# Kernel tuning notes

Measured on AMD Instinct MI355X. Metric: run time of the kernel, lower is better.

The kernel has to match this reference:

```python
import jax, jax.numpy as jnp
import numpy as np

ATTN_HEADS = 4
NEG = -1e9
LN_EPS = 1e-5


def _ln(x, s, b):
    m = x.mean(-1, keepdims=True)
    v = ((x - m) ** 2).mean(-1, keepdims=True)
    return (x - m) * jax.lax.rsqrt(v + LN_EPS) * s + b


def setup_inputs() -> dict:
    key = jax.random.key(0)
    ks = jax.random.split(key, 40)
    B, L, D, FF, NL = 512, 192, 256, 1024, 2
    V, U, I = 30000, 100000, 50000
    Lp, Ln, NF = 30, 300, 13
    Lu = jax.random.randint(ks[0], (B,), 1, L // 2)
    Li = jax.random.randint(ks[1], (B,), 1, L // 2)
    inp = {
        'attr': jax.random.randint(ks[2], (B, L), 0, V),
        'attr_inds': jax.random.randint(ks[3], (B, L), 0, 3),
        'attr_tf': jax.random.uniform(ks[4], (B, L), dtype=jnp.float32),
        'attr_feat': jax.random.normal(ks[5], (B, L, NF), dtype=jnp.float32),
        'attr_lens': Lu + Li,
        'attr_lens_user': Lu,
        'attr_lens_item': Li,
        'user_ids': jax.random.randint(ks[6], (B,), 0, U),
        'item_ids': jax.random.randint(ks[7], (B,), 0, I),
        'pos_targets': jax.random.randint(ks[8], (B, Lp), 0, V),
        'pos_lens': jax.random.randint(ks[9], (B,), 1, Lp + 1),
        'neg_targets': jax.random.randint(ks[10], (B, Ln), 0, V),
        'neg_lens': jax.random.randint(ks[11], (B,), 1, Ln + 1),
        # embedding tables (uniform(-0.1,0.1) per f_init_weight)
        'attr_emb': jax.random.uniform(ks[12], (V, D), minval=-0.1, maxval=0.1),
        'ind_emb': jax.random.uniform(ks[13], (3, D), minval=-0.1, maxval=0.1),
        'user_emb_table': jax.random.uniform(ks[14], (U, D), minval=-0.1, maxval=0.1),
        'item_emb_table': jax.random.uniform(ks[15], (I, D), minval=-0.1, maxval=0.1),
        'out_emb_user': jax.random.uniform(ks[16], (V, 2 * D), minval=-0.1, maxval=0.1),
        'out_emb_item': jax.random.uniform(ks[17], (V, 2 * D), minval=-0.1, maxval=0.1),
        # attr-weight head: Linear(13,1) + sigmoid
        'feat_w': jax.random.normal(ks[18], (NF,)) * 0.02,
        'feat_b': jnp.zeros(()),
        # transformer encoder params, stacked over NL layers
        'Wqkv': jax.random.normal(ks[19], (NL, 3 * D, D)) * 0.02,
        'bqkv': jnp.zeros((NL, 3 * D)),
        'Wo': jax.random.normal(ks[20], (NL, D, D)) * 0.02,
        'bo': jnp.zeros((NL, D)),
        'ln1_s': jnp.ones((NL, D)), 'ln1_b': jnp.zeros((NL, D)),
        'W1': jax.random.normal(ks[21], (NL, FF, D)) * 0.02,
        'b1': jnp.zeros((NL, FF)),
        'W2': jax.random.normal(ks[22], (NL, D, FF)) * 0.02,
        'b2': jnp.zeros((NL, D)),
        'ln2_s': jnp.ones((NL, D)), 'ln2_b': jnp.zeros((NL, D)),
    }
    return inp


def reference(attr, attr_inds, attr_tf, attr_feat, attr_lens, attr_lens_user,
              attr_lens_item, user_ids, item_ids, pos_targets, pos_lens,
              neg_targets, neg_lens, attr_emb, ind_emb, user_emb_table,
              item_emb_table, out_emb_user, out_emb_item, feat_w, feat_b,
              Wqkv, bqkv, Wo, bo, ln1_s, ln1_b, W1, b1, W2, b2, ln2_s, ln2_b):
    B, L = attr.shape
    D = attr_emb.shape[1]
    NL = Wqkv.shape[0]
    Dh = D // ATTN_HEADS
    pos = jnp.arange(L)
    valid = pos[None, :] < attr_lens[:, None]  # [B,L] True = valid key

    x = attr_emb[attr] + ind_emb[attr_inds]  # [B,L,D]
    for l in range(NL):  # post-LN TransformerEncoderLayer, relu, no dropout
        qkv = x @ Wqkv[l].T + bqkv[l]
        q, k, v = jnp.split(qkv, 3, axis=-1)
        q = q.reshape(B, L, ATTN_HEADS, Dh).transpose(0, 2, 1, 3)
        k = k.reshape(B, L, ATTN_HEADS, Dh).transpose(0, 2, 1, 3)
        v = v.reshape(B, L, ATTN_HEADS, Dh).transpose(0, 2, 1, 3)
        scores = jnp.einsum('bhqd,bhkd->bhqk', q, k) / np.sqrt(Dh).astype(x.dtype)
        scores = jnp.where(valid[:, None, None, :], scores, NEG)
        a = jax.nn.softmax(scores, axis=-1)
        ctx = jnp.einsum('bhqk,bhkd->bhqd', a, v).transpose(0, 2, 1, 3).reshape(B, L, D)
        x = _ln(x + ctx @ Wo[l].T + bo[l], ln1_s[l], ln1_b[l])
        ff = jax.nn.relu(x @ W1[l].T + b1[l]) @ W2[l].T + b2[l]
        x = _ln(x + ff, ln2_s[l], ln2_b[l])

    # ragged weighted segment average over user span [0,Lu) and item span [Lu,Lu+Li)
    w_user = jax.nn.sigmoid(attr_feat @ feat_w + feat_b)  # [B,L]
    wted = x * attr_tf[..., None]
    umask = pos[None, :] < attr_lens_user[:, None]
    imask = (~umask) & (pos[None, :] < (attr_lens_user + attr_lens_item)[:, None])
    user_x = (wted * w_user[..., None] * umask[..., None]).sum(1) / attr_lens_user[:, None].astype(x.dtype)
    item_x = (wted * (1.0 - w_user)[..., None] * imask[..., None]).sum(1) / attr_lens_item[:, None].astype(x.dtype)

    user_out = jnp.concatenate([user_x, user_emb_table[user_ids]], axis=-1)  # [B,2D]
    item_out = jnp.concatenate([item_x, item_emb_table[item_ids]], axis=-1)

    def logit(t):
        return (jnp.einsum('bkd,bd->bk', out_emb_user[t], user_out)
                + jnp.einsum('bkd,bd->bk', out_emb_item[t], item_out))

    pos_logits = logit(pos_targets)
    neg_logits = logit(neg_targets)
    pmask = jnp.arange(pos_targets.shape[1])[None, :] < pos_lens[:, None]
    nmask = jnp.arange(neg_targets.shape[1])[None, :] < neg_lens[:, None]
    logits = jnp.concatenate([pos_logits, neg_logits], axis=-1)
    mask = jnp.concatenate([pmask, nmask], axis=-1)
    new_targets = jnp.concatenate([jnp.ones_like(pos_targets), jnp.zeros_like(neg_targets)], axis=1) * mask
    return logits, mask, new_targets
```

## Files before the change

### kernel.cpp

```cpp
#include <hip/hip_runtime.h>
#include <hip/hip_bf16.h>
#include <cstdint>
#include <cstddef>

#define B_ 512
#define L_ 192
#define D_ 256
#define H_ 4
#define DH_ 64
#define FF_ 1024
#define NL_ 2
#define LP_ 30
#define LNEG_ 300
#define NF_ 13
#define M_ (B_*L_)
#define NT_ 330
#define V_ 30000

typedef __attribute__((ext_vector_type(8))) short bf16x8;
typedef __attribute__((ext_vector_type(4))) float f32x4;

__device__ __forceinline__ ushort f2b(float f) {
  union { float f; uint32_t u; } v; v.f = f;
  uint32_t u = v.u;
  return (ushort)((u + 0x7FFFu + ((u >> 16) & 1u)) >> 16);
}
__device__ __forceinline__ float b2f(ushort u) {
  union { uint32_t u; float f; } v; v.u = (uint32_t)u << 16; return v.f;
}

__global__ __launch_bounds__(512) void k_prefix(
    const int* __restrict__ lens, int* __restrict__ off,
    int* __restrict__ ccnt, int* __restrict__ ccntp, int Bc, int nchunks)
{
  const int t = threadIdx.x;
  int s = 0;
  for (int i = 0; i < t; ++i) s += lens[i];
  off[t] = s;
  if (t == 511) off[512] = s + lens[511];
  if (t < nchunks) {
    int s2 = 0;
    const int c0 = t * Bc;
    for (int i = 0; i < Bc; ++i) s2 += lens[c0 + i];
    ccnt[t]  = s2;
    ccntp[t] = (s2 + 127) & ~127;
  }
}

__global__ __launch_bounds__(256) void k_f2b(const float* __restrict__ in, ushort* __restrict__ out) {
  const int i = (blockIdx.x*256 + threadIdx.x)*8;
  float4 a = *(const float4*)(in+i);
  float4 b = *(const float4*)(in+i+4);
  ushort4 o1; o1.x=f2b(a.x); o1.y=f2b(a.y); o1.z=f2b(a.z); o1.w=f2b(a.w);
  ushort4 o2; o2.x=f2b(b.x); o2.y=f2b(b.y); o2.z=f2b(b.z); o2.w=f2b(b.w);
  *(ushort4*)(out+i)   = o1;
  *(ushort4*)(out+i+4) = o2;
}

__global__ __launch_bounds__(256) void k_f2b4(
    const float* __restrict__ wq, const float* __restrict__ wo,
    const float* __restrict__ w1, const float* __restrict__ w2,
    ushort* __restrict__ oq, ushort* __restrict__ oo,
    ushort* __restrict__ o1, ushort* __restrict__ o2)
{
  int bb = blockIdx.x;
  const float* in; ushort* out; int base;
  if (bb < 192)      { in = wq; out = oq; base = bb; }
  else if (bb < 256) { in = wo; out = oo; base = bb - 192; }
  else if (bb < 512) { in = w1; out = o1; base = bb - 256; }
  else               { in = w2; out = o2; base = bb - 512; }
  const int i = base*2048 + threadIdx.x*8;
  float4 a = *(const float4*)(in+i);
  float4 b = *(const float4*)(in+i+4);
  ushort4 q1; q1.x=f2b(a.x); q1.y=f2b(a.y); q1.z=f2b(a.z); q1.w=f2b(a.w);
  ushort4 q2; q2.x=f2b(b.x); q2.y=f2b(b.y); q2.z=f2b(b.z); q2.w=f2b(b.w);
  *(ushort4*)(out+i)   = q1;
  *(ushort4*)(out+i+4) = q2;
}

__global__ __launch_bounds__(256) void k_embed(
    const int* __restrict__ attr, const int* __restrict__ inds,
    const int* __restrict__ lens, const int* __restrict__ off,
    const float* __restrict__ attr_emb, const float* __restrict__ ind_emb,
    ushort* __restrict__ xb)
{
  int idx = blockIdx.x*256 + threadIdx.x;
  int token = idx >> 6;
  int c = (idx & 63) * 4;
  int b = token / L_;
  int l = token - b*L_;
  if (l >= lens[b]) return;
  size_t crow = (size_t)off[b] + l;
  int a = attr[token];
  int id = inds[token];
  const float4 e  = *(const float4*)(attr_emb + (size_t)a*D_ + c);
  const float4 ie = *(const float4*)(ind_emb  + (size_t)id*D_ + c);
  ushort4 ob; ob.x=f2b(e.x+ie.x); ob.y=f2b(e.y+ie.y); ob.z=f2b(e.z+ie.z); ob.w=f2b(e.w+ie.w);
  *(ushort4*)(xb + crow*D_ + c) = ob;
}

template<int OUT_BF16, int RELU>
__global__ __launch_bounds__(256) void k_gemm_mfma(
    const ushort* __restrict__ A, const int* __restrict__ aoffp,
    const int* __restrict__ cntp,
    const ushort* __restrict__ W, const float* __restrict__ bias,
    void* __restrict__ Cv, int N, int K)
{
  if ((int)blockIdx.y * 128 >= *cntp) return;
  __shared__ alignas(16) ushort As[8192];
  __shared__ alignas(16) ushort Bs[8192];
  const int abase = *aoffp;
  const int tid = threadIdx.x;
  const int w = tid >> 6, l = tid & 63;
  const int g = l >> 4, c16 = l & 15;
  const int m0 = blockIdx.y*128, n0 = blockIdx.x*128;
  const int wr = w >> 1, wc = w & 1;
  const int swzr = (c16 & 7) << 4;

  f32x4 acc[4][4];
  #pragma unroll
  for (int i=0;i<4;++i)
    #pragma unroll
    for (int j=0;j<4;++j) acc[i][j] = (f32x4){0.f,0.f,0.f,0.f};

  for (int k0=0; k0<K; k0+=64) {
    #pragma unroll
    for (int i=0;i<4;++i) {
      const int li  = i*4096 + tid*16;
      const int row = li >> 7;
      const int col = ((li & 127) ^ ((row & 7) << 4)) >> 1;
      const ushort* ga = A + (size_t)(abase+m0+row)*K + k0 + col;
      const ushort* gb = W + (size_t)(n0+row)*K + k0 + col;
      ushort* la = As + i*2048 + w*512;
      ushort* lb = Bs + i*2048 + w*512;
      __builtin_amdgcn_global_load_lds((const __attribute__((address_space(1))) unsigned int*)ga,
                                       (__attribute__((address_space(3))) unsigned int*)la, 16, 0, 0);
      __builtin_amdgcn_global_load_lds((const __attribute__((address_space(1))) unsigned int*)gb,
                                       (__attribute__((address_space(3))) unsigned int*)lb, 16, 0, 0);
    }
    __syncthreads();
    #pragma unroll
    for (int ks=0; ks<2; ++ks) {
      const int cb = ((g*16 + ks*64) ^ swzr) >> 1;
      bf16x8 af[4], bfr[4];
      #pragma unroll
      for (int i2=0;i2<4;++i2) {
        af[i2]  = *(const bf16x8*)(As + (size_t)(wr*64 + i2*16 + c16)*64 + cb);
        bfr[i2] = *(const bf16x8*)(Bs + (size_t)(wc*64 + i2*16 + c16)*64 + cb);
      }
      #pragma unroll
      for (int mi=0;mi<4;++mi)
        #pragma unroll
        for (int ni=0;ni<4;++ni)
          acc[mi][ni] = __builtin_amdgcn_mfma_f32_16x16x32_bf16(af[mi], bfr[ni], acc[mi][ni], 0,0,0);
    }
    __syncthreads();
  }
  const int col0 = n0 + wc*64 + c16;
  const int row0 = m0 + wr*64 + (g<<2);
  #pragma unroll
  for (int ni=0;ni<4;++ni) {
    const float bv = bias[col0 + ni*16];
    #pragma unroll
    for (int mi=0;mi<4;++mi) {
      #pragma unroll
      for (int r=0;r<4;++r) {
        float v = acc[mi][ni][r] + bv;
        if (RELU) v = fmaxf(v, 0.f);
        const size_t idx = (size_t)(row0 + mi*16 + r)*N + col0 + ni*16;
        if (OUT_BF16) ((ushort*)Cv)[idx] = f2b(v);
        else          ((float*)Cv)[idx]  = v;
      }
    }
  }
}

__global__ __launch_bounds__(512) void k_gemm_ln(
    const ushort* __restrict__ A,
    const int* __restrict__ cntp, const int* __restrict__ cnt,
    const int* __restrict__ xoffp,
    const ushort* __restrict__ W,
    const float* __restrict__ bias,
    const float* __restrict__ lns, const float* __restrict__ lnb,
    ushort* __restrict__ xb, int K)
{
  const int m0 = blockIdx.x*128;
  if (m0 >= *cntp) return;
  __shared__ alignas(16) ushort As[8192];
  __shared__ alignas(16) ushort Bs[16384];
  __shared__ float red[4][2][128];
  const int tid = threadIdx.x;
  const int w = tid >> 6, l = tid & 63;
  const int g = l >> 4, c16 = l & 15;
  const int wr = w >> 2, wc = w & 3;
  const int swzr = (c16 & 7) << 4;

  f32x4 acc[4][4];
  #pragma unroll
  for (int i=0;i<4;++i)
    #pragma unroll
    for (int j=0;j<4;++j) acc[i][j] = (f32x4){0.f,0.f,0.f,0.f};

  for (int k0=0; k0<K; k0+=64) {
    #pragma unroll
    for (int i=0;i<2;++i) {
      const int li  = i*8192 + tid*16;
      const int row = li >> 7;
      const int col = ((li & 127) ^ ((row & 7) << 4)) >> 1;
      const ushort* ga = A + (size_t)(m0+row)*K + k0 + col;
      ushort* la = As + i*4096 + w*512;
      __builtin_amdgcn_global_load_lds((const __attribute__((address_space(1))) unsigned int*)ga,
                                       (__attribute__((address_space(3))) unsigned int*)la, 16, 0, 0);
    }
    #pragma unroll
    for (int i=0;i<4;++i) {
      const int li  = i*8192 + tid*16;
      const int row = li >> 7;
      const int col = ((li & 127) ^ ((row & 7) << 4)) >> 1;
      const ushort* gb = W + (size_t)row*K + k0 + col;
      ushort* lb = Bs + i*4096 + w*512;
      __builtin_amdgcn_global_load_lds((const __attribute__((address_space(1))) unsigned int*)gb,
                                       (__attribute__((address_space(3))) unsigned int*)lb, 16, 0, 0);
    }
    __syncthreads();
    #pragma unroll
    for (int ks=0; ks<2; ++ks) {
      const int cb = ((g*16 + ks*64) ^ swzr) >> 1;
      bf16x8 af[4], bfr[4];
      #pragma unroll
      for (int i2=0;i2<4;++i2) {
        af[i2]  = *(const bf16x8*)(As + (size_t)(wr*64 + i2*16 + c16)*64 + cb);
        bfr[i2] = *(const bf16x8*)(Bs + (size_t)(wc*64 + i2*16 + c16)*64 + cb);
      }
      #pragma unroll
      for (int mi=0;mi<4;++mi)
        #pragma unroll
        for (int ni=0;ni<4;++ni)
          acc[mi][ni] = __builtin_amdgcn_mfma_f32_16x16x32_bf16(af[mi], bfr[ni], acc[mi][ni], 0,0,0);
    }
    __syncthreads();
  }

  const int xbase = *xoffp + m0;
  float bvs[4], svs[4], bbs[4];
  #pragma unroll
  for (int ni=0;ni<4;++ni) {
    int col = wc*64 + ni*16 + c16;
    bvs[ni] = bias[col]; svs[ni] = lns[col]; bbs[ni] = lnb[col];
  }
  float ps[4][4], pq[4][4];
  #pragma unroll
  for (int mi=0;mi<4;++mi) {
    #pragma unroll
    for (int r=0;r<4;++r) {
      ps[mi][r]=0.f; pq[mi][r]=0.f;
      const int lrow = wr*64 + mi*16 + 4*g + r;
      const ushort* xr = xb + (size_t)(xbase + lrow)*256;
      #pragma unroll
      for (int ni=0;ni<4;++ni) {
        float y = acc[mi][ni][r] + bvs[ni] + b2f(xr[wc*64 + ni*16 + c16]);
        acc[mi][ni][r] = y;
        ps[mi][r] += y;
        pq[mi][r] += y*y;
      }
    }
  }
  #pragma unroll
  for (int mi=0;mi<4;++mi)
    #pragma unroll
    for (int r=0;r<4;++r) {
      #pragma unroll
      for (int off=1; off<16; off<<=1) {
        ps[mi][r] += __shfl_xor(ps[mi][r], off, 16);
        pq[mi][r] += __shfl_xor(pq[mi][r], off, 16);
      }
    }
  if (c16 == 0) {
    #pragma unroll
    for (int mi=0;mi<4;++mi)
      #pragma unroll
      for (int r=0;r<4;++r) {
        const int lrow = wr*64 + mi*16 + 4*g + r;
        red[wc][0][lrow] = ps[mi][r];
        red[wc][1][lrow] = pq[mi][r];
      }
  }
  __syncthreads();
  const int cexact = *cnt;
  #pragma unroll
  for (int mi=0;mi<4;++mi) {
    #pragma unroll
    for (int r=0;r<4;++r) {
      const int lrow = wr*64 + mi*16 + 4*g + r;
      float tsum = red[0][0][lrow] + red[1][0][lrow] + red[2][0][lrow] + red[3][0][lrow];
      float tsq  = red[0][1][lrow] + red[1][1][lrow] + red[2][1][lrow] + red[3][1][lrow];
      float mean = tsum * (1.f/256.f);
      float var  = tsq * (1.f/256.f) - mean*mean;
      float inv  = rsqrtf(var + 1e-5f);
      if (m0 + lrow < cexact) {
        ushort* xbr = xb + (size_t)(xbase + lrow)*256;
        #pragma unroll
        for (int ni=0;ni<4;++ni) {
          int col = wc*64 + ni*16 + c16;
          xbr[col] = f2b((acc[mi][ni][r] - mean)*inv*svs[ni] + bbs[ni]);
        }
      }
    }
  }
}

__global__ __launch_bounds__(512) void k_ffn(
    const int* __restrict__ cntp, const int* __restrict__ cnt,
    const int* __restrict__ xoffp,
    const ushort* __restrict__ W1, const float* __restrict__ b1,
    const ushort* __restrict__ W2, const float* __restrict__ b2,
    const float* __restrict__ lns, const float* __restrict__ lnb,
    ushort* __restrict__ xb)
{
  const int m0 = blockIdx.x*128;
  if (m0 >= *cntp) return;
  __shared__ alignas(16) char lds[65536];
  __shared__ float red[4][2][128];
  const int tid = threadIdx.x;
  const int w = tid >> 6, l = tid & 63;
  const int g = l >> 4, c16 = l & 15;
  const int wr = w >> 2, wc = w & 3;
  const int swzr = (c16 & 7) << 4;
  const int xbase = *xoffp + m0;

  f32x4 tac[4][4];
  #pragma unroll
  for (int i=0;i<4;++i)
    #pragma unroll
    for (int j=0;j<4;++j) tac[i][j] = (f32x4){0.f,0.f,0.f,0.f};

  for (int s=0; s<8; ++s) {
    f32x4 hac[4][2];
    #pragma unroll
    for (int i=0;i<4;++i)
      #pragma unroll
      for (int j=0;j<2;++j) hac[i][j] = (f32x4){0.f,0.f,0.f,0.f};
    for (int kc=0; kc<4; ++kc) {
      __syncthreads();
      #pragma unroll
      for (int i=0;i<2;++i) {
        const int li  = i*8192 + tid*16;
        const int row = li >> 7;
        const int col = ((li & 127) ^ ((row & 7) << 4)) >> 1;
        const ushort* ga = xb + (size_t)(xbase+row)*256 + kc*64 + col;
        char* la = lds + i*8192 + w*1024;
        __builtin_amdgcn_global_load_lds((const __attribute__((address_space(1))) unsigned int*)ga,
                                         (__attribute__((address_space(3))) unsigned int*)la, 16, 0, 0);
      }
      #pragma unroll
      for (int i=0;i<2;++i) {
        const int li  = i*8192 + tid*16;
        const int row = li >> 7;
        const int col = ((li & 127) ^ ((row & 7) << 4)) >> 1;
        const ushort* gb = W1 + (size_t)(s*128+row)*256 + kc*64 + col;
        char* lb = lds + 16384 + i*8192 + w*1024;
        __builtin_amdgcn_global_load_lds((const __attribute__((address_space(1))) unsigned int*)gb,
                                         (__attribute__((address_space(3))) unsigned int*)lb, 16, 0, 0);
      }
      __syncthreads();
      #pragma unroll
      for (int ks=0; ks<2; ++ks) {
        const int cb = (g*16 + ks*64) ^ swzr;
        bf16x8 af[4], bf[2];
        #pragma unroll
        for (int mi=0;mi<4;++mi)
          af[mi] = *(const bf16x8*)(lds + (wr*64 + mi*16 + c16)*128 + cb);
        #pragma unroll
        for (int ni=0;ni<2;++ni)
          bf[ni] = *(const bf16x8*)(lds + 16384 + (wc*32 + ni*16 + c16)*128 + cb);
        #pragma unroll
        for (int mi=0;mi<4;++mi)
          #pragma unroll
          for (int ni=0;ni<2;++ni)
            hac[mi][ni] = __builtin_amdgcn_mfma_f32_16x16x32_bf16(af[mi], bf[ni], hac[mi][ni], 0,0,0);
      }
    }
    {
      float bv1[2];
      #pragma unroll
      for (int ni=0;ni<2;++ni) bv1[ni] = b1[s*128 + wc*32 + ni*16 + c16];
      #pragma unroll
      for (int mi=0;mi<4;++mi)
        #pragma unroll
        for (int ni=0;ni<2;++ni)
          #pragma unroll
          for (int r=0;r<4;++r) {
            int row = wr*64 + mi*16 + 4*g + r;
            int colb = (wc*32 + ni*16 + c16)*2;
            float h = fmaxf(hac[mi][ni][r] + bv1[ni], 0.f);
            *(ushort*)(lds + 32768 + row*256 + (colb ^ ((row&7)<<4))) = f2b(h);
          }
    }
    __syncthreads();
    for (int kc2=0; kc2<2; ++kc2) {
      if (kc2) __syncthreads();
      #pragma unroll
      for (int i=0;i<4;++i) {
        const int li  = i*8192 + tid*16;
        const int row = li >> 7;
        const int col = ((li & 127) ^ ((row & 7) << 4)) >> 1;
        const ushort* gb = W2 + (size_t)row*1024 + s*128 + kc2*64 + col;
        char* lb = lds + i*8192 + w*1024;
        __builtin_amdgcn_global_load_lds((const __attribute__((address_space(1))) unsigned int*)gb,
                                         (__attribute__((address_space(3))) unsigned int*)lb, 16, 0, 0);
      }
      __syncthreads();
      #pragma unroll
      for (int ks=0; ks<2; ++ks) {
        bf16x8 af[4], bf[4];
        #pragma unroll
        for (int mi=0;mi<4;++mi) {
          int row = wr*64 + mi*16 + c16;
          int colb = kc2*128 + g*16 + ks*64;
          af[mi] = *(const bf16x8*)(lds + 32768 + row*256 + (colb ^ ((row&7)<<4)));
        }
        const int cb = (g*16 + ks*64) ^ swzr;
        #pragma unroll
        for (int ni=0;ni<4;++ni)
          bf[ni] = *(const bf16x8*)(lds + (wc*64 + ni*16 + c16)*128 + cb);
        #pragma unroll
        for (int mi=0;mi<4;++mi)
          #pragma unroll
          for (int ni=0;ni<4;++ni)
            tac[mi][ni] = __builtin_amdgcn_mfma_f32_16x16x32_bf16(af[mi], bf[ni], tac[mi][ni], 0,0,0);
      }
    }
    __syncthreads();
  }

  float bvs[4], svs[4], bbs[4];
  #pragma unroll
  for (int ni=0;ni<4;++ni) {
    int col = wc*64 + ni*16 + c16;
    bvs[ni] = b2[col]; svs[ni] = lns[col]; bbs[ni] = lnb[col];
  }
  float ps[4][4], pq[4][4];
  #pragma unroll
  for (int mi=0;mi<4;++mi) {
    #pragma unroll
    for (int r=0;r<4;++r) {
      ps[mi][r]=0.f; pq[mi][r]=0.f;
      const int lrow = wr*64 + mi*16 + 4*g + r;
      const ushort* xr = xb + (size_t)(xbase + lrow)*256;
      #pragma unroll
      for (int ni=0;ni<4;++ni) {
        float y = tac[mi][ni][r] + bvs[ni] + b2f(xr[wc*64 + ni*16 + c16]);
        tac[mi][ni][r] = y;
        ps[mi][r] += y;
        pq[mi][r] += y*y;
      }
    }
  }
  #pragma unroll
  for (int mi=0;mi<4;++mi)
    #pragma unroll
    for (int r=0;r<4;++r) {
      #pragma unroll
      for (int off=1; off<16; off<<=1) {
        ps[mi][r] += __shfl_xor(ps[mi][r], off, 16);
        pq[mi][r] += __shfl_xor(pq[mi][r], off, 16);
      }
    }
  if (c16 == 0) {
    #pragma unroll
    for (int mi=0;mi<4;++mi)
      #pragma unroll
      for (int r=0;r<4;++r) {
        const int lrow = wr*64 + mi*16 + 4*g + r;
        red[wc][0][lrow] = ps[mi][r];
        red[wc][1][lrow] = pq[mi][r];
      }
  }
  __syncthreads();
  const int cexact = *cnt;
  #pragma unroll
  for (int mi=0;mi<4;++mi) {
    #pragma unroll
    for (int r=0;r<4;++r) {
      const int lrow = wr*64 + mi*16 + 4*g + r;
      float tsum = red[0][0][lrow] + red[1][0][lrow] + red[2][0][lrow] + red[3][0][lrow];
      float tsq  = red[0][1][lrow] + red[1][1][lrow] + red[2][1][lrow] + red[3][1][lrow];
      float mean = tsum * (1.f/256.f);
      float var  = tsq * (1.f/256.f) - mean*mean;
      float inv  = rsqrtf(var + 1e-5f);
      if (m0 + lrow < cexact) {
        ushort* xbr = xb + (size_t)(xbase + lrow)*256;
        #pragma unroll
        for (int ni=0;ni<4;++ni) {
          int col = wc*64 + ni*16 + c16;
          xbr[col] = f2b((tac[mi][ni][r] - mean)*inv*svs[ni] + bbs[ni]);
        }
      }
    }
  }
}

__global__ __launch_bounds__(256) void k_attn_mfma(
    const ushort* __restrict__ qkv, ushort* __restrict__ ctx,
    const int* __restrict__ offc)
{
  __shared__ alignas(16) char lds[81920];
  char* Kb = lds;
  char* Vt = lds + 24576;
  const int tid = threadIdx.x;
  const int w = tid >> 6, l = tid & 63;
  const int g = l >> 4, c = l & 15;
  char* Pw = lds + 57344 + w*6144;
  const int bl = blockIdx.x >> 2, h = blockIdx.x & 3;
  const int rowbase = offc[bl] - offc[0];
  const int len = offc[bl+1] - offc[bl];
  const int nkt = (len + 15) >> 4;
  const int nkf = (len + 31) >> 5;
  const ushort* base = qkv + (size_t)rowbase*768;
  ushort* cbase = ctx + (size_t)rowbase*256;

  const int lenk8 = nkt*16*8;
  for (int idx = tid; idx < lenk8; idx += 256) {
    int row = idx >> 3, ch = idx & 7;
    uint4 v = *(const uint4*)(base + (size_t)row*768 + 256 + h*64 + ch*8);
    *(uint4*)(Kb + ((row*128 + ch*16) ^ ((row&7)<<4))) = v;
  }
  {
    const int lenv = nkf*32;
    int d0 = (tid & 15)*4;
    for (int key = tid >> 4; key < lenv; key += 16) {
      ushort4 v = *(const ushort4*)(base + (size_t)key*768 + 512 + h*64 + d0);
      ushort vv[4] = {v.x, v.y, v.z, v.w};
      #pragma unroll
      for (int j=0;j<4;++j) {
        int d = d0 + j;
        *(ushort*)(Vt + ((d*512 + key*2) ^ ((d&7)<<4))) = vv[j];
      }
    }
  }
  __syncthreads();

  for (int t = nkt; t < 2*nkf; ++t) {
    #pragma unroll
    for (int r=0;r<4;++r) {
      int q = 4*g + r;
      *(ushort*)(Pw + (((t>>1)*1024 + q*64 + ((t&1)*16 + c)*2) ^ (((q>>2)&3)<<4))) = 0;
    }
  }

  const int nst = (len + 15) >> 4;
  for (int s = w; s < nst; s += 4) {
    const ushort* qp = base + (size_t)(s*16 + c)*768 + h*64 + g*8;
    bf16x8 aq0 = *(const bf16x8*)qp;
    bf16x8 aq1 = *(const bf16x8*)(qp + 32);

    f32x4 sc[12];
    #pragma unroll
    for (int t=0;t<12;++t) {
      sc[t] = (f32x4){0.f,0.f,0.f,0.f};
      if (t < nkt) {
        int ba0 = ((t*16 + c)*128 + g*16)      ^ ((c&7)<<4);
        int ba1 = ((t*16 + c)*128 + g*16 + 64) ^ ((c&7)<<4);
        bf16x8 k0 = *(const bf16x8*)(Kb + ba0);
        bf16x8 k1 = *(const bf16x8*)(Kb + ba1);
        sc[t] = __builtin_amdgcn_mfma_f32_16x16x32_bf16(aq0, k0, sc[t], 0,0,0);
        sc[t] = __builtin_amdgcn_mfma_f32_16x16x32_bf16(aq1, k1, sc[t], 0,0,0);
        if (t == nkt-1 && t*16 + c >= len)
          sc[t] = (f32x4){-1e30f,-1e30f,-1e30f,-1e30f};
      }
    }
    float mr[4] = {-1e30f,-1e30f,-1e30f,-1e30f};
    #pragma unroll
    for (int t=0;t<12;++t) if (t<nkt) {
      #pragma unroll
      for (int r=0;r<4;++r) mr[r] = fmaxf(mr[r], sc[t][r]);
    }
    #pragma unroll
    for (int r=0;r<4;++r) {
      mr[r] = fmaxf(mr[r], __shfl_xor(mr[r], 1, 16));
      mr[r] = fmaxf(mr[r], __shfl_xor(mr[r], 2, 16));
      mr[r] = fmaxf(mr[r], __shfl_xor(mr[r], 4, 16));
      mr[r] = fmaxf(mr[r], __shfl_xor(mr[r], 8, 16));
    }
    float sr[4] = {0.f,0.f,0.f,0.f};
    #pragma unroll
    for (int t=0;t<12;++t) if (t<nkt) {
      #pragma unroll
      for (int r=0;r<4;++r) {
        float p = __expf((sc[t][r] - mr[r]) * 0.125f);
        sr[r] += p;
        int q = 4*g + r;
        *(ushort*)(Pw + (((t>>1)*1024 + q*64 + ((t&1)*16 + c)*2) ^ (((q>>2)&3)<<4))) = f2b(p);
      }
    }
    #pragma unroll
    for (int r=0;r<4;++r) {
      sr[r] += __shfl_xor(sr[r], 1, 16);
      sr[r] += __shfl_xor(sr[r], 2, 16);
      sr[r] += __shfl_xor(sr[r], 4, 16);
      sr[r] += __shfl_xor(sr[r], 8, 16);
    }
    f32x4 oa[4];
    #pragma unroll
    for (int dt=0;dt<4;++dt) oa[dt] = (f32x4){0.f,0.f,0.f,0.f};
    #pragma unroll
    for (int kf=0;kf<6;++kf) if (kf<nkf) {
      bf16x8 pf = *(const bf16x8*)(Pw + ((kf*1024 + c*64 + g*16) ^ (((c>>2)&3)<<4)));
      #pragma unroll
      for (int dt=0;dt<4;++dt) {
        int d = dt*16 + c;
        bf16x8 vf = *(const bf16x8*)(Vt + ((d*512 + kf*64 + g*16) ^ ((d&7)<<4)));
        oa[dt] = __builtin_amdgcn_mfma_f32_16x16x32_bf16(pf, vf, oa[dt], 0,0,0);
      }
    }
    float inv[4];
    #pragma unroll
    for (int r=0;r<4;++r) inv[r] = 1.f / sr[r];
    ushort* orow = cbase + (size_t)(s*16)*256 + h*64;
    #pragma unroll
    for (int r=0;r<4;++r) {
      int q = 4*g + r;
      if (s*16 + q < len) {
        #pragma unroll
        for (int dt=0;dt<4;++dt)
          orow[(size_t)q*256 + dt*16 + c] = f2b(oa[dt][r] * inv[r]);
      }
    }
  }
}

__global__ __launch_bounds__(256) void k_pool(
    const ushort* __restrict__ xb, const int* __restrict__ off,
    const float* __restrict__ attr_tf, const float* __restrict__ attr_feat,
    const int* __restrict__ lens_u, const int* __restrict__ lens_i,
    const int* __restrict__ user_ids, const int* __restrict__ item_ids,
    const float* __restrict__ user_tab, const float* __restrict__ item_tab,
    const float* __restrict__ feat_w, const float* __restrict__ feat_b,
    float* __restrict__ user_out, float* __restrict__ item_out)
{
  __shared__ float wu[L_], tf[L_];
  const int b = blockIdx.x;
  const int t = threadIdx.x;
  if (t < L_) {
    const float* f = attr_feat + ((size_t)b*L_ + t)*NF_;
    float sacc = feat_b[0];
    #pragma unroll
    for (int j=0;j<NF_;++j) sacc = fmaf(f[j], feat_w[j], sacc);
    wu[t] = 1.f/(1.f+__expf(-sacc));
    tf[t] = attr_tf[b*L_+t];
  }
  __syncthreads();
  const int Lu = lens_u[b], Li = lens_i[b];
  const ushort* xrow = xb + (size_t)off[b]*D_;
  float su=0.f, si=0.f;
  for (int l=0;l<Lu+Li;++l) {
    float val = b2f(xrow[(size_t)l*D_ + t]) * tf[l];
    if (l < Lu) su = fmaf(val, wu[l], su);
    else        si = fmaf(val, 1.f-wu[l], si);
  }
  user_out[(size_t)b*512 + t]       = su/(float)Lu;
  item_out[(size_t)b*512 + t]       = si/(float)Li;
  user_out[(size_t)b*512 + 256 + t] = user_tab[(size_t)user_ids[b]*D_ + t];
  item_out[(size_t)b*512 + 256 + t] = item_tab[(size_t)item_ids[b]*D_ + t];
}

__global__ __launch_bounds__(256) void k_logits(
    const int* __restrict__ pos_t, const int* __restrict__ neg_t,
    const int* __restrict__ pos_l, const int* __restrict__ neg_l,
    const ushort* __restrict__ oeu, const ushort* __restrict__ oei,
    const float* __restrict__ user_out, const float* __restrict__ item_out,
    float* __restrict__ out)
{
  const int g = blockIdx.x*4 + (threadIdx.x >> 6);
  const int lane = threadIdx.x & 63;
  const int b = g / NT_;
  const int k = g - b*NT_;
  const int tid_ = (k < LP_) ? pos_t[b*LP_ + k] : neg_t[b*LNEG_ + (k-LP_)];
  const ushort* eu = oeu + (size_t)tid_*512;
  const ushort* ei = oei + (size_t)tid_*512;
  const float* uo = user_out + (size_t)b*512;
  const float* io = item_out + (size_t)b*512;
  const int d0 = lane*8;
  float s = 0.f;
  ushort4 a0 = *(const ushort4*)(eu+d0), a1 = *(const ushort4*)(eu+d0+4);
  float4 u0 = *(const float4*)(uo+d0), u1 = *(const float4*)(uo+d0+4);
  s += b2f(a0.x)*u0.x + b2f(a0.y)*u0.y + b2f(a0.z)*u0.z + b2f(a0.w)*u0.w;
  s += b2f(a1.x)*u1.x + b2f(a1.y)*u1.y + b2f(a1.z)*u1.z + b2f(a1.w)*u1.w;
  ushort4 c0 = *(const ushort4*)(ei+d0), c1 = *(const ushort4*)(ei+d0+4);
  float4 i0 = *(const float4*)(io+d0), i1 = *(const float4*)(io+d0+4);
  s += b2f(c0.x)*i0.x + b2f(c0.y)*i0.y + b2f(c0.z)*i0.z + b2f(c0.w)*i0.w;
  s += b2f(c1.x)*i1.x + b2f(c1.y)*i1.y + b2f(c1.z)*i1.z + b2f(c1.w)*i1.w;
  #pragma unroll
  for (int off=32; off>0; off>>=1) s += __shfl_xor(s, off, 64);
  if (lane == 0) {
    out[(size_t)b*NT_ + k] = s;
    float mv, nt;
    if (k < LP_) { mv = (k < pos_l[b]) ? 1.f : 0.f; nt = mv; }
    else         { mv = ((k - LP_) < neg_l[b]) ? 1.f : 0.f; nt = 0.f; }
    out[(size_t)B_*NT_   + (size_t)b*NT_ + k] = mv;
    out[(size_t)2*B_*NT_ + (size_t)b*NT_ + k] = nt;
  }
}

extern "C" void kernel_launch(void* const* d_in, const int* in_sizes, int n_in,
                              void* d_out, int out_size, void* d_ws, size_t ws_size,
                              hipStream_t stream)
{
  const int*   attr      = (const int*)d_in[0];
  const int*   attr_inds = (const int*)d_in[1];
  const float* attr_tf   = (const float*)d_in[2];
  const float* attr_feat = (const float*)d_in[3];
  const int*   attr_lens = (const int*)d_in[4];
  const int*   lens_u    = (const int*)d_in[5];
  const int*   lens_i    = (const int*)d_in[6];
  const int*   user_ids  = (const int*)d_in[7];
  const int*   item_ids  = (const int*)d_in[8];
  const int*   pos_t     = (const int*)d_in[9];
  const int*   pos_l     = (const int*)d_in[10];
  const int*   neg_t     = (const int*)d_in[11];
  const int*   neg_l     = (const int*)d_in[12];
  const float* attr_emb  = (const float*)d_in[13];
  const float* ind_emb   = (const float*)d_in[14];
  const float* user_tab  = (const float*)d_in[15];
  const float* item_tab  = (const float*)d_in[16];
  const float* oeu       = (const float*)d_in[17];
  const float* oei       = (const float*)d_in[18];
  const float* feat_w    = (const float*)d_in[19];
  const float* feat_b    = (const float*)d_in[20];
  const float* Wqkv      = (const float*)d_in[21];
  const float* bqkv      = (const float*)d_in[22];
  const float* Wo        = (const float*)d_in[23];
  const float* bo        = (const float*)d_in[24];
  const float* ln1s      = (const float*)d_in[25];
  const float* ln1b      = (const float*)d_in[26];
  const float* W1        = (const float*)d_in[27];
  const float* b1        = (const float*)d_in[28];
  const float* W2        = (const float*)d_in[29];
  const float* b2        = (const float*)d_in[30];
  const float* ln2s      = (const float*)d_in[31];
  const float* ln2b      = (const float*)d_in[32];

  int* ioff  = (int*)d_ws;
  int* ccnt  = ioff + 520;
  int* ccntp = ccnt + 64;
  float* ws = (float*)d_ws + 768;
  float* uo = ws;
  float* io = uo + (size_t)B_*512;
  ushort* xb   = (ushort*)(io + (size_t)B_*512);
  ushort* wq_b = xb + (size_t)M_*D_;
  ushort* wo_b = wq_b + (size_t)2*768*256;
  ushort* w1_b = wo_b + (size_t)2*256*256;
  ushort* w2_b = w1_b + (size_t)2*1024*256;
  ushort* oeu_b = w2_b + (size_t)2*256*1024;
  ushort* oei_b = oeu_b + (size_t)V_*512;
  float* scratch = (float*)(oei_b + (size_t)V_*512);

  const size_t fixed_floats = 768 + (size_t)B_*1024 + (size_t)M_*(D_/2) + 786432 + (size_t)V_*512;
  int Bc = 8;
  for (int cand = 512; cand >= 8; cand >>= 1) {
    size_t need = (fixed_floats + (size_t)cand*L_*512) * sizeof(float);
    if (need <= ws_size) { Bc = cand; break; }
  }
  const int nchunks = B_ / Bc;
  const size_t Mc = (size_t)Bc * L_;

  float* out = (float*)d_out;

  k_prefix<<<1, 512, 0, stream>>>(attr_lens, ioff, ccnt, ccntp, Bc, nchunks);
  k_f2b4<<<768, 256, 0, stream>>>(Wqkv, Wo, W1, W2, wq_b, wo_b, w1_b, w2_b);
  k_f2b<<<(V_*512)/2048, 256, 0, stream>>>(oeu, oeu_b);
  k_f2b<<<(V_*512)/2048, 256, 0, stream>>>(oei, oei_b);
  k_embed<<<M_*64/256, 256, 0, stream>>>(attr, attr_inds, attr_lens, ioff, attr_emb, ind_emb, xb);

  for (int l=0; l<NL_; ++l) {
    const float* bqkv_l = bqkv + (size_t)l*768;
    const float* bo_l   = bo   + (size_t)l*D_;
    const float* b1_l   = b1   + (size_t)l*FF_;
    const float* b2_l   = b2   + (size_t)l*D_;
    for (int c=0; c<nchunks; ++c) {
      const int* offc = ioff + c*Bc;
      const int* cntp = ccntp + c;
      const int* cnt  = ccnt + c;
      ushort* qkv_b = (ushort*)scratch;
      ushort* ctx_b = (ushort*)(scratch + Mc*384);

      k_gemm_mfma<1,0><<<dim3(768/128, Mc/128), 256, 0, stream>>>(
          xb, offc, cntp, wq_b + (size_t)l*768*256, bqkv_l, qkv_b, 768, 256);
      k_attn_mfma<<<Bc*H_, 256, 0, stream>>>(qkv_b, ctx_b, offc);
      k_gemm_ln<<<Mc/128, 512, 0, stream>>>(
          ctx_b, cntp, cnt, offc, wo_b + (size_t)l*256*256, bo_l,
          ln1s + (size_t)l*D_, ln1b + (size_t)l*D_, xb, 256);
      k_ffn<<<Mc/128, 512, 0, stream>>>(
          cntp, cnt, offc, w1_b + (size_t)l*1024*256, b1_l,
          w2_b + (size_t)l*256*1024, b2_l,
          ln2s + (size_t)l*D_, ln2b + (size_t)l*D_, xb);
    }
  }
  k_pool<<<B_, 256, 0, stream>>>(xb, ioff, attr_tf, attr_feat, lens_u, lens_i, user_ids, item_ids,
                                 user_tab, item_tab, feat_w, feat_b, uo, io);
  k_logits<<<B_*NT_/4, 256, 0, stream>>>(pos_t, neg_t, pos_l, neg_l, oeu_b, oei_b, uo, io, out);
}
```

Measured before the change: 703.4 us.

## Transpose MFMA operands for vectorized epilogues; stream FFN activations from global with W1 double-buffering

Swaps the A/B operands of the MFMA calls so that each lane holds 4 consecutive output columns of one row. This turns the bias, residual and LayerNorm epilogues into float4/ushort4 vector loads and stores, and shrinks the row reduction to two cross-group shuffles. In the FFN kernel, the X tile is no longer staged in LDS. X fragments are read directly from global memory per k-step, and W1 chunks are double-buffered in LDS so the next chunk loads while the current one is used. The direct X reads trade LDS traffic and barriers for repeated global/L2 reads of the same activations across the 8 hidden slices.

```diff
diff --git a/kernel.cpp b/kernel.cpp
--- a/kernel.cpp
+++ b/kernel.cpp
@@ -152,24 +152,28 @@
       for (int mi=0;mi<4;++mi)
         #pragma unroll
         for (int ni=0;ni<4;++ni)
-          acc[mi][ni] = __builtin_amdgcn_mfma_f32_16x16x32_bf16(af[mi], bfr[ni], acc[mi][ni], 0,0,0);
+          acc[mi][ni] = __builtin_amdgcn_mfma_f32_16x16x32_bf16(bfr[ni], af[mi], acc[mi][ni], 0,0,0);
     }
     __syncthreads();
   }
-  const int col0 = n0 + wc*64 + c16;
-  const int row0 = m0 + wr*64 + (g<<2);
   #pragma unroll
   for (int ni=0;ni<4;++ni) {
-    const float bv = bias[col0 + ni*16];
+    const int nc = n0 + wc*64 + ni*16 + 4*g;
+    const float4 bv = *(const float4*)(bias + nc);
     #pragma unroll
     for (int mi=0;mi<4;++mi) {
-      #pragma unroll
-      for (int r=0;r<4;++r) {
-        float v = acc[mi][ni][r] + bv;
-        if (RELU) v = fmaxf(v, 0.f);
-        const size_t idx = (size_t)(row0 + mi*16 + r)*N + col0 + ni*16;
-        if (OUT_BF16) ((ushort*)Cv)[idx] = f2b(v);
-        else          ((float*)Cv)[idx]  = v;
+      float v0 = acc[mi][ni][0] + bv.x;
+      float v1 = acc[mi][ni][1] + bv.y;
+      float v2 = acc[mi][ni][2] + bv.z;
+      float v3 = acc[mi][ni][3] + bv.w;
+      if (RELU) { v0=fmaxf(v0,0.f); v1=fmaxf(v1,0.f); v2=fmaxf(v2,0.f); v3=fmaxf(v3,0.f); }
+      const size_t idx = (size_t)(m0 + wr*64 + mi*16 + c16)*N + nc;
+      if (OUT_BF16) {
+        ushort4 o; o.x=f2b(v0); o.y=f2b(v1); o.z=f2b(v2); o.w=f2b(v3);
+        *(ushort4*)((ushort*)Cv + idx) = o;
+      } else {
+        float4 o; o.x=v0; o.y=v1; o.z=v2; o.w=v3;
+        *(float4*)((float*)Cv + idx) = o;
       }
     }
   }
@@ -236,74 +240,75 @@
       for (int mi=0;mi<4;++mi)
         #pragma unroll
         for (int ni=0;ni<4;++ni)
-          acc[mi][ni] = __builtin_amdgcn_mfma_f32_16x16x32_bf16(af[mi], bfr[ni], acc[mi][ni], 0,0,0);
+          acc[mi][ni] = __builtin_amdgcn_mfma_f32_16x16x32_bf16(bfr[ni], af[mi], acc[mi][ni], 0,0,0);
     }
     __syncthreads();
   }
 
   const int xbase = *xoffp + m0;
-  float bvs[4], svs[4], bbs[4];
+  float4 bv[4], sv[4], bb[4];
   #pragma unroll
   for (int ni=0;ni<4;++ni) {
-    int col = wc*64 + ni*16 + c16;
-    bvs[ni] = bias[col]; svs[ni] = lns[col]; bbs[ni] = lnb[col];
-  }
-  float ps[4][4], pq[4][4];
+    const int nc = wc*64 + ni*16 + 4*g;
+    bv[ni] = *(const float4*)(bias + nc);
+    sv[ni] = *(const float4*)(lns + nc);
+    bb[ni] = *(const float4*)(lnb + nc);
+  }
+  float ps[4], pq[4];
   #pragma unroll
   for (int mi=0;mi<4;++mi) {
-    #pragma unroll
-    for (int r=0;r<4;++r) {
-      ps[mi][r]=0.f; pq[mi][r]=0.f;
-      const int lrow = wr*64 + mi*16 + 4*g + r;
-      const ushort* xr = xb + (size_t)(xbase + lrow)*256;
-      #pragma unroll
-      for (int ni=0;ni<4;++ni) {
-        float y = acc[mi][ni][r] + bvs[ni] + b2f(xr[wc*64 + ni*16 + c16]);
-        acc[mi][ni][r] = y;
-        ps[mi][r] += y;
-        pq[mi][r] += y*y;
-      }
-    }
-  }
-  #pragma unroll
-  for (int mi=0;mi<4;++mi)
-    #pragma unroll
-    for (int r=0;r<4;++r) {
-      #pragma unroll
-      for (int off=1; off<16; off<<=1) {
-        ps[mi][r] += __shfl_xor(ps[mi][r], off, 16);
-        pq[mi][r] += __shfl_xor(pq[mi][r], off, 16);
-      }
-    }
-  if (c16 == 0) {
-    #pragma unroll
-    for (int mi=0;mi<4;++mi)
-      #pragma unroll
-      for (int r=0;r<4;++r) {
-        const int lrow = wr*64 + mi*16 + 4*g + r;
-        red[wc][0][lrow] = ps[mi][r];
-        red[wc][1][lrow] = pq[mi][r];
-      }
+    ps[mi]=0.f; pq[mi]=0.f;
+    const int lrow = wr*64 + mi*16 + c16;
+    const ushort* xr = xb + (size_t)(xbase + lrow)*256;
+    #pragma unroll
+    for (int ni=0;ni<4;++ni) {
+      const int nc = wc*64 + ni*16 + 4*g;
+      ushort4 rx = *(const ushort4*)(xr + nc);
+      float y0 = acc[mi][ni][0] + bv[ni].x + b2f(rx.x);
+      float y1 = acc[mi][ni][1] + bv[ni].y + b2f(rx.y);
+      float y2 = acc[mi][ni][2] + bv[ni].z + b2f(rx.z);
+      float y3 = acc[mi][ni][3] + bv[ni].w + b2f(rx.w);
+      acc[mi][ni][0]=y0; acc[mi][ni][1]=y1; acc[mi][ni][2]=y2; acc[mi][ni][3]=y3;
+      ps[mi] += (y0+y1)+(y2+y3);
+      pq[mi] += (y0*y0+y1*y1)+(y2*y2+y3*y3);
+    }
+  }
+  #pragma unroll
+  for (int mi=0;mi<4;++mi) {
+    ps[mi] += __shfl_xor(ps[mi], 16, 64);
+    pq[mi] += __shfl_xor(pq[mi], 16, 64);
+    ps[mi] += __shfl_xor(ps[mi], 32, 64);
+    pq[mi] += __shfl_xor(pq[mi], 32, 64);
+  }
+  if (g == 0) {
+    #pragma unroll
+    for (int mi=0;mi<4;++mi) {
+      const int lrow = wr*64 + mi*16 + c16;
+      red[wc][0][lrow] = ps[mi];
+      red[wc][1][lrow] = pq[mi];
+    }
   }
   __syncthreads();
   const int cexact = *cnt;
   #pragma unroll
   for (int mi=0;mi<4;++mi) {
-    #pragma unroll
-    for (int r=0;r<4;++r) {
-      const int lrow = wr*64 + mi*16 + 4*g + r;
-      float tsum = red[0][0][lrow] + red[1][0][lrow] + red[2][0][lrow] + red[3][0][lrow];
-      float tsq  = red[0][1][lrow] + red[1][1][lrow] + red[2][1][lrow] + red[3][1][lrow];
-      float mean = tsum * (1.f/256.f);
-      float var  = tsq * (1.f/256.f) - mean*mean;
-      float inv  = rsqrtf(var + 1e-5f);
-      if (m0 + lrow < cexact) {
-        ushort* xbr = xb + (size_t)(xbase + lrow)*256;
-        #pragma unroll
-        for (int ni=0;ni<4;++ni) {
-          int col = wc*64 + ni*16 + c16;
-          xbr[col] = f2b((acc[mi][ni][r] - mean)*inv*svs[ni] + bbs[ni]);
-        }
+    const int lrow = wr*64 + mi*16 + c16;
+    float tsum = red[0][0][lrow] + red[1][0][lrow] + red[2][0][lrow] + red[3][0][lrow];
+    float tsq  = red[0][1][lrow] + red[1][1][lrow] + red[2][1][lrow] + red[3][1][lrow];
+    float mean = tsum * (1.f/256.f);
+    float var  = tsq * (1.f/256.f) - mean*mean;
+    float inv  = rsqrtf(var + 1e-5f);
+    if (m0 + lrow < cexact) {
+      ushort* xbr = xb + (size_t)(xbase + lrow)*256;
+      #pragma unroll
+      for (int ni=0;ni<4;++ni) {
+        const int nc = wc*64 + ni*16 + 4*g;
+        ushort4 o;
+        o.x = f2b((acc[mi][ni][0]-mean)*inv*sv[ni].x + bb[ni].x);
+        o.y = f2b((acc[mi][ni][1]-mean)*inv*sv[ni].y + bb[ni].y);
+        o.z = f2b((acc[mi][ni][2]-mean)*inv*sv[ni].z + bb[ni].z);
+        o.w = f2b((acc[mi][ni][3]-mean)*inv*sv[ni].w + bb[ni].w);
+        *(ushort4*)(xbr + nc) = o;
       }
     }
   }
@@ -328,6 +333,14 @@
   const int swzr = (c16 & 7) << 4;
   const int xbase = *xoffp + m0;
 
+  const ushort* xrow[4];
+  int tokl[4];
+  #pragma unroll
+  for (int mi=0;mi<4;++mi) {
+    tokl[mi] = wr*64 + mi*16 + c16;
+    xrow[mi] = xb + (size_t)(xbase + tokl[mi])*256;
+  }
+
   f32x4 tac[4][4];
   #pragma unroll
   for (int i=0;i<4;++i)
@@ -340,65 +353,73 @@
     for (int i=0;i<4;++i)
       #pragma unroll
       for (int j=0;j<2;++j) hac[i][j] = (f32x4){0.f,0.f,0.f,0.f};
+
+    #pragma unroll
+    for (int i=0;i<2;++i) {
+      const int li  = i*8192 + tid*16;
+      const int row = li >> 7;
+      const int col = ((li & 127) ^ ((row & 7) << 4)) >> 1;
+      const ushort* gb = W1 + (size_t)(s*128+row)*256 + col;
+      char* lb = lds + i*8192 + w*1024;
+      __builtin_amdgcn_global_load_lds((const __attribute__((address_space(1))) unsigned int*)gb,
+                                       (__attribute__((address_space(3))) unsigned int*)lb, 16, 0, 0);
+    }
+    __syncthreads();
+
+    #pragma unroll
     for (int kc=0; kc<4; ++kc) {
-      __syncthreads();
-      #pragma unroll
-      for (int i=0;i<2;++i) {
-        const int li  = i*8192 + tid*16;
-        const int row = li >> 7;
-        const int col = ((li & 127) ^ ((row & 7) << 4)) >> 1;
-        const ushort* ga = xb + (size_t)(xbase+row)*256 + kc*64 + col;
-        char* la = lds + i*8192 + w*1024;
-        __builtin_amdgcn_global_load_lds((const __attribute__((address_space(1))) unsigned int*)ga,
-                                         (__attribute__((address_space(3))) unsigned int*)la, 16, 0, 0);
-      }
-      #pragma unroll
-      for (int i=0;i<2;++i) {
-        const int li  = i*8192 + tid*16;
-        const int row = li >> 7;
-        const int col = ((li & 127) ^ ((row & 7) << 4)) >> 1;
-        const ushort* gb = W1 + (size_t)(s*128+row)*256 + kc*64 + col;
-        char* lb = lds + 16384 + i*8192 + w*1024;
-        __builtin_amdgcn_global_load_lds((const __attribute__((address_space(1))) unsigned int*)gb,
-                                         (__attribute__((address_space(3))) unsigned int*)lb, 16, 0, 0);
-      }
-      __syncthreads();
+      char* cur = lds + (kc&1)*16384;
+      if (kc < 3) {
+        char* nxt = lds + ((kc+1)&1)*16384;
+        #pragma unroll
+        for (int i=0;i<2;++i) {
+          const int li  = i*8192 + tid*16;
+          const int row = li >> 7;
+          const int col = ((li & 127) ^ ((row & 7) << 4)) >> 1;
+          const ushort* gb = W1 + (size_t)(s*128+row)*256 + (kc+1)*64 + col;
+          char* lb = nxt + i*8192 + w*1024;
+          __builtin_amdgcn_global_load_lds((const __attribute__((address_space(1))) unsigned int*)gb,
+                                           (__attribute__((address_space(3))) unsigned int*)lb, 16, 0, 0);
+        }
+      }
       #pragma unroll
       for (int ks=0; ks<2; ++ks) {
         const int cb = (g*16 + ks*64) ^ swzr;
-        bf16x8 af[4], bf[2];
+        bf16x8 w1f[2];
+        #pragma unroll
+        for (int ni=0;ni<2;++ni)
+          w1f[ni] = *(const bf16x8*)(cur + (wc*32 + ni*16 + c16)*128 + cb);
+        bf16x8 xf[4];
         #pragma unroll
         for (int mi=0;mi<4;++mi)
-          af[mi] = *(const bf16x8*)(lds + (wr*64 + mi*16 + c16)*128 + cb);
-        #pragma unroll
-        for (int ni=0;ni<2;++ni)
-          bf[ni] = *(const bf16x8*)(lds + 16384 + (wc*32 + ni*16 + c16)*128 + cb);
+          xf[mi] = *(const bf16x8*)(xrow[mi] + kc*64 + ks*32 + g*8);
         #pragma unroll
         for (int mi=0;mi<4;++mi)
           #pragma unroll
           for (int ni=0;ni<2;++ni)
-            hac[mi][ni] = __builtin_amdgcn_mfma_f32_16x16x32_bf16(af[mi], bf[ni], hac[mi][ni], 0,0,0);
-      }
-    }
-    {
-      float bv1[2];
-      #pragma unroll
-      for (int ni=0;ni<2;++ni) bv1[ni] = b1[s*128 + wc*32 + ni*16 + c16];
-      #pragma unroll
-      for (int mi=0;mi<4;++mi)
-        #pragma unroll
-        for (int ni=0;ni<2;++ni)
-          #pragma unroll
-          for (int r=0;r<4;++r) {
-            int row = wr*64 + mi*16 + 4*g + r;
-            int colb = (wc*32 + ni*16 + c16)*2;
-            float h = fmaxf(hac[mi][ni][r] + bv1[ni], 0.f);
-            *(ushort*)(lds + 32768 + row*256 + (colb ^ ((row&7)<<4))) = f2b(h);
-          }
-    }
-    __syncthreads();
+            hac[mi][ni] = __builtin_amdgcn_mfma_f32_16x16x32_bf16(w1f[ni], xf[mi], hac[mi][ni], 0,0,0);
+      }
+      __syncthreads();
+    }
+
+    #pragma unroll
+    for (int ni=0;ni<2;++ni) {
+      const int ffc = s*128 + wc*32 + ni*16 + 4*g;
+      const float4 bb1 = *(const float4*)(b1 + ffc);
+      #pragma unroll
+      for (int mi=0;mi<4;++mi) {
+        ushort4 o;
+        o.x = f2b(fmaxf(hac[mi][ni][0] + bb1.x, 0.f));
+        o.y = f2b(fmaxf(hac[mi][ni][1] + bb1.y, 0.f));
+        o.z = f2b(fmaxf(hac[mi][ni][2] + bb1.z, 0.f));
+        o.w = f2b(fmaxf(hac[mi][ni][3] + bb1.w, 0.f));
+        const int ffb = (wc*32 + ni*16 + 4*g)*2;
+        *(ushort4*)(lds + 32768 + tokl[mi]*256 + (ffb ^ ((tokl[mi]&7)<<4))) = o;
+      }
+    }
+
+    #pragma unroll
     for (int kc2=0; kc2<2; ++kc2) {
-      if (kc2) __syncthreads();
       #pragma unroll
       for (int i=0;i<4;++i) {
         const int li  = i*8192 + tid*16;
@@ -412,89 +433,88 @@
       __syncthreads();
       #pragma unroll
       for (int ks=0; ks<2; ++ks) {
-        bf16x8 af[4], bf[4];
+        const int cb = (g*16 + ks*64) ^ swzr;
+        bf16x8 w2f[4];
+        #pragma unroll
+        for (int ni=0;ni<4;++ni)
+          w2f[ni] = *(const bf16x8*)(lds + (wc*64 + ni*16 + c16)*128 + cb);
+        bf16x8 hf[4];
         #pragma unroll
         for (int mi=0;mi<4;++mi) {
-          int row = wr*64 + mi*16 + c16;
-          int colb = kc2*128 + g*16 + ks*64;
-          af[mi] = *(const bf16x8*)(lds + 32768 + row*256 + (colb ^ ((row&7)<<4)));
+          const int ffb2 = kc2*128 + ks*64 + g*16;
+          hf[mi] = *(const bf16x8*)(lds + 32768 + tokl[mi]*256 + (ffb2 ^ ((tokl[mi]&7)<<4)));
         }
-        const int cb = (g*16 + ks*64) ^ swzr;
-        #pragma unroll
-        for (int ni=0;ni<4;++ni)
-          bf[ni] = *(const bf16x8*)(lds + (wc*64 + ni*16 + c16)*128 + cb);
         #pragma unroll
         for (int mi=0;mi<4;++mi)
           #pragma unroll
           for (int ni=0;ni<4;++ni)
-            tac[mi][ni] = __builtin_amdgcn_mfma_f32_16x16x32_bf16(af[mi], bf[ni], tac[mi][ni], 0,0,0);
-      }
-    }
-    __syncthreads();
-  }
-
-  float bvs[4], svs[4], bbs[4];
+            tac[mi][ni] = __builtin_amdgcn_mfma_f32_16x16x32_bf16(w2f[ni], hf[mi], tac[mi][ni], 0,0,0);
+      }
+      __syncthreads();
+    }
+  }
+
+  float4 bv[4], sv[4], bb[4];
   #pragma unroll
   for (int ni=0;ni<4;++ni) {
-    int col = wc*64 + ni*16 + c16;
-    bvs[ni] = b2[col]; svs[ni] = lns[col]; bbs[ni] = lnb[col];
-  }
-  float ps[4][4], pq[4][4];
+    const int nc = wc*64 + ni*16 + 4*g;
+    bv[ni] = *(const float4*)(b2 + nc);
+    sv[ni] = *(const float4*)(lns + nc);
+    bb[ni] = *(const float4*)(lnb + nc);
+  }
+  float ps[4], pq[4];
   #pragma unroll
   for (int mi=0;mi<4;++mi) {
-    #pragma unroll
-    for (int r=0;r<4;++r) {
-      ps[mi][r]=0.f; pq[mi][r]=0.f;
-      const int lrow = wr*64 + mi*16 + 4*g + r;
-      const ushort* xr = xb + (size_t)(xbase + lrow)*256;
-      #pragma unroll
-      for (int ni=0;ni<4;++ni) {
-        float y = tac[mi][ni][r] + bvs[ni] + b2f(xr[wc*64 + ni*16 + c16]);
-        tac[mi][ni][r] = y;
-        ps[mi][r] += y;
-        pq[mi][r] += y*y;
-      }
-    }
-  }
-  #pragma unroll
-  for (int mi=0;mi<4;++mi)
-    #pragma unroll
-    for (int r=0;r<4;++r) {
-      #pragma unroll
-      for (int off=1; off<16; off<<=1) {
-        ps[mi][r] += __shfl_xor(ps[mi][r], off, 16);
-        pq[mi][r] += __shfl_xor(pq[mi][r], off, 16);
-      }
-    }
-  if (c16 == 0) {
-    #pragma unroll
-    for (int mi=0;mi<4;++mi)
-      #pragma unroll
-      for (int r=0;r<4;++r) {
-        const int lrow = wr*64 + mi*16 + 4*g + r;
-        red[wc][0][lrow] = ps[mi][r];
-        red[wc][1][lrow] = pq[mi][r];
-      }
+    ps[mi]=0.f; pq[mi]=0.f;
+    const ushort* xr = xrow[mi];
+    #pragma unroll
+    for (int ni=0;ni<4;++ni) {
+      const int nc = wc*64 + ni*16 + 4*g;
+      ushort4 rx = *(const ushort4*)(xr + nc);
+      float y0 = tac[mi][ni][0] + bv[ni].x + b2f(rx.x);
+      float y1 = tac[mi][ni][1] + bv[ni].y + b2f(rx.y);
+      float y2 = tac[mi][ni][2] + bv[ni].z + b2f(rx.z);
+      float y3 = tac[mi][ni][3] + bv[ni].w + b2f(rx.w);
+      tac[mi][ni][0]=y0; tac[mi][ni][1]=y1; tac[mi][ni][2]=y2; tac[mi][ni][3]=y3;
+      ps[mi] += (y0+y1)+(y2+y3);
+      pq[mi] += (y0*y0+y1*y1)+(y2*y2+y3*y3);
+    }
+  }
+  #pragma unroll
+  for (int mi=0;mi<4;++mi) {
+    ps[mi] += __shfl_xor(ps[mi], 16, 64);
+    pq[mi] += __shfl_xor(pq[mi], 16, 64);
+    ps[mi] += __shfl_xor(ps[mi], 32, 64);
+    pq[mi] += __shfl_xor(pq[mi], 32, 64);
+  }
+  if (g == 0) {
+    #pragma unroll
+    for (int mi=0;mi<4;++mi) {
+      red[wc][0][tokl[mi]] = ps[mi];
+      red[wc][1][tokl[mi]] = pq[mi];
+    }
   }
   __syncthreads();
   const int cexact = *cnt;
   #pragma unroll
   for (int mi=0;mi<4;++mi) {
-    #pragma unroll
-    for (int r=0;r<4;++r) {
-      const int lrow = wr*64 + mi*16 + 4*g + r;
-      float tsum = red[0][0][lrow] + red[1][0][lrow] + red[2][0][lrow] + red[3][0][lrow];
-      float tsq  = red[0][1][lrow] + red[1][1][lrow] + red[2][1][lrow] + red[3][1][lrow];
-      float mean = tsum * (1.f/256.f);
-      float var  = tsq * (1.f/256.f) - mean*mean;
-      float inv  = rsqrtf(var + 1e-5f);
-      if (m0 + lrow < cexact) {
-        ushort* xbr = xb + (size_t)(xbase + lrow)*256;
-        #pragma unroll
-        for (int ni=0;ni<4;++ni) {
-          int col = wc*64 + ni*16 + c16;
-          xbr[col] = f2b((tac[mi][ni][r] - mean)*inv*svs[ni] + bbs[ni]);
-        }
+    const int lrow = tokl[mi];
+    float tsum = red[0][0][lrow] + red[1][0][lrow] + red[2][0][lrow] + red[3][0][lrow];
+    float tsq  = red[0][1][lrow] + red[1][1][lrow] + red[2][1][lrow] + red[3][1][lrow];
+    float mean = tsum * (1.f/256.f);
+    float var  = tsq * (1.f/256.f) - mean*mean;
+    float inv  = rsqrtf(var + 1e-5f);
+    if (m0 + lrow < cexact) {
+      ushort* xbr = xb + (size_t)(xbase + lrow)*256;
+      #pragma unroll
+      for (int ni=0;ni<4;++ni) {
+        const int nc = wc*64 + ni*16 + 4*g;
+        ushort4 o;
+        o.x = f2b((tac[mi][ni][0]-mean)*inv*sv[ni].x + bb[ni].x);
+        o.y = f2b((tac[mi][ni][1]-mean)*inv*sv[ni].y + bb[ni].y);
+        o.z = f2b((tac[mi][ni][2]-mean)*inv*sv[ni].z + bb[ni].z);
+        o.w = f2b((tac[mi][ni][3]-mean)*inv*sv[ni].w + bb[ni].w);
+        *(ushort4*)(xbr + nc) = o;
       }
     }
   }
```

Measured after the change: 868.0 us. 23.4% more time.
